# Kernel tuning notes

Hardware: AMD Instinct MI355X
Metric: run time of the kernel (lower is better)

Reference implementation:

```python
import jax, jax.numpy as jnp
import numpy as np
from jax import lax

B, L, D, N, DFF = 2, 2048, 1024, 16, 4096
EPS = 1e-6


def _phi1(z):
    # (exp(z) - 1) / z with stable limit 1 at z -> 0
    small = jnp.abs(z) < 1e-4
    zs = jnp.where(small, 1.0, z)
    return jnp.where(small, 1.0 + 0.5 * z, jnp.expm1(zs) / zs)


def _rmsnorm(x, w):
    return x * lax.rsqrt(jnp.mean(x * x, axis=-1, keepdims=True) + EPS) * w


def setup_inputs() -> dict:
    key = jax.random.key(0)
    ks = jax.random.split(key, 16)
    s_in = 0.02
    return {
        "x": jax.random.normal(ks[0], (B, L, D), jnp.float32),
        "norm1_w": jnp.ones((D,), jnp.float32),
        "norm2_w": jnp.ones((D,), jnp.float32),
        "A_log": jnp.log(jnp.arange(1, N + 1, dtype=jnp.float32)),  # A = -exp(A_log)
        "D_param": jnp.ones((D,), jnp.float32),
        "scale": jnp.ones((D,), jnp.float32),
        "Wdt": jax.random.normal(ks[1], (D, D), jnp.float32) * s_in,
        "bdt": jnp.zeros((D,), jnp.float32),
        "WB": jax.random.normal(ks[2], (N, D), jnp.float32) * s_in,
        "bB": jnp.zeros((N,), jnp.float32),
        "WC": jax.random.normal(ks[3], (N, D), jnp.float32) * s_in,
        "bC": jnp.zeros((N,), jnp.float32),
        "W1": jax.random.normal(ks[4], (DFF, D), jnp.float32) * s_in,
        "b1": jnp.zeros((DFF,), jnp.float32),
        "W2": jax.random.normal(ks[5], (D, DFF), jnp.float32) * s_in,
        "b2": jnp.zeros((D,), jnp.float32),
    }


def _mamba(xn, A_log, D_param, scale, Wdt, bdt, WB, bB, WC, bC):
    # xn: (B, L, D)
    A = -jnp.exp(A_log)  # (N,)
    dt = jax.nn.softplus(xn @ Wdt.T + bdt)      # (B, L, D)
    Bv = xn @ WB.T + bB                          # (B, L, N)
    Cv = xn @ WC.T + bC                          # (B, L, N)
    dtA = dt[..., None] * A                      # (B, L, D, N)
    dA = jnp.exp(dtA)                            # (B, L, D, N)
    b = _phi1(dtA) * Bv[:, :, None, :] * xn[..., None]  # (B, L, D, N)

    def step(h, inp):
        dA_t, b_t = inp
        h = dA_t * h + b_t
        return h, h

    h0 = jnp.zeros((xn.shape[0], xn.shape[2], A.shape[0]), xn.dtype)
    _, h_traj = lax.scan(step, h0, (jnp.moveaxis(dA, 1, 0), jnp.moveaxis(b, 1, 0)))
    h_traj = jnp.moveaxis(h_traj, 0, 1)          # (B, L, D, N)
    y = jnp.einsum('bln,bldn->bld', Cv, h_traj) + D_param * xn
    return y * scale


def reference(x, norm1_w, norm2_w, A_log, D_param, scale, Wdt, bdt, WB, bB, WC, bC, W1, b1, W2, b2):
    res = x
    xn = _rmsnorm(x, norm1_w)
    x = _mamba(xn, A_log, D_param, scale, Wdt, bdt, WB, bB, WC, bC) + res
    res = x
    xn = _rmsnorm(x, norm2_w)
    h = jax.nn.gelu(xn @ W1.T + b1, approximate=True)
    x = h @ W2.T + b2 + res
    return x
```

## Files before the change

kernel.cpp:

```cpp
#include <hip/hip_runtime.h>


#define GLOBAL_AS __attribute__((address_space(1)))
#define LDS_AS __attribute__((address_space(3)))

typedef __attribute__((ext_vector_type(8))) short short8;
typedef __attribute__((ext_vector_type(4))) float f32x4;

static constexpr int Bc = 2, Lc = 2048, Dc = 1024, Nc = 16, DFFc = 4096;
static constexpr int BL = Bc * Lc;
static constexpr int CHUNK = 32, NCHUNK = 64;
static constexpr int NP = 1152;

__device__ __forceinline__ float bf2f(unsigned short u) {
    return __uint_as_float(((unsigned)u) << 16);
}
__device__ __forceinline__ unsigned short f2bf(float f) {
    unsigned u = __float_as_uint(f);
    u += 0x7fff + ((u >> 16) & 1);
    return (unsigned short)(u >> 16);
}

static constexpr int NCVT = NP * Dc + DFFc * Dc + Dc * DFFc;
static constexpr int NCVT_BLK = NCVT / 4 / 256;
__global__ __launch_bounds__(256) void cvt_rms(const float* __restrict__ Wdt,
                                               const float* __restrict__ WB,
                                               const float* __restrict__ WC,
                                               const float* __restrict__ W1,
                                               const float* __restrict__ W2,
                                               unsigned short* __restrict__ wcomb,
                                               unsigned short* __restrict__ w1b,
                                               unsigned short* __restrict__ w2b,
                                               const float* __restrict__ x,
                                               const float* __restrict__ n1w,
                                               unsigned short* __restrict__ xn1) {
    const int tid = threadIdx.x;
    if (blockIdx.x < NCVT_BLK) {
        constexpr int n0 = Dc * Dc;
        constexpr int n1 = Nc * Dc;
        constexpr int n2 = Nc * Dc;
        constexpr int n3 = 96 * Dc;
        constexpr int nC = n0 + n1 + n2 + n3;
        constexpr int n4 = DFFc * Dc;
        constexpr int n5 = Dc * DFFc;
        static_assert(nC == NP * Dc, "pad mismatch");
        const int i = (blockIdx.x * 256 + tid) * 4;
        const float* s;
        unsigned short* d;
        if (i < n0)                 { s = Wdt + i;             d = wcomb + i; }
        else if (i < n0 + n1)       { s = WB + (i - n0);       d = wcomb + i; }
        else if (i < n0 + n1 + n2)  { s = WC + (i - n0 - n1);  d = wcomb + i; }
        else if (i < nC)            { *(ushort4*)(wcomb + i) = ushort4{0, 0, 0, 0}; return; }
        else if (i < nC + n4)       { s = W1 + (i - nC);       d = w1b + (i - nC); }
        else if (i < nC + n4 + n5)  { s = W2 + (i - nC - n4);  d = w2b + (i - nC - n4); }
        else return;
        float4 v = *(const float4*)s;
        ushort4 o;
        o.x = f2bf(v.x); o.y = f2bf(v.y); o.z = f2bf(v.z); o.w = f2bf(v.w);
        *(ushort4*)d = o;
        return;
    }
    const int row = blockIdx.x - NCVT_BLK;
    float4 v = ((const float4*)(x + (size_t)row * Dc))[tid];
    float ss = v.x * v.x + v.y * v.y + v.z * v.z + v.w * v.w;
#pragma unroll
    for (int off = 32; off > 0; off >>= 1) ss += __shfl_down(ss, off, 64);
    __shared__ float red[4];
    if ((tid & 63) == 0) red[tid >> 6] = ss;
    __syncthreads();
    float tot = red[0] + red[1] + red[2] + red[3];
    float rs = rsqrtf(tot * (1.0f / Dc) + 1e-6f);
    float4 wv = ((const float4*)n1w)[tid];
    ushort4 o;
    o.x = f2bf(v.x * rs * wv.x); o.y = f2bf(v.y * rs * wv.y);
    o.z = f2bf(v.z * rs * wv.z); o.w = f2bf(v.w * rs * wv.w);
    ((ushort4*)(xn1 + (size_t)row * Dc))[tid] = o;
}

__global__ __launch_bounds__(256) void rmsnorm_k(const float* __restrict__ x,
                                                 const float* __restrict__ w,
                                                 unsigned short* __restrict__ out) {
    const int row = blockIdx.x, tid = threadIdx.x;
    float4 v = ((const float4*)(x + (size_t)row * Dc))[tid];
    float ss = v.x * v.x + v.y * v.y + v.z * v.z + v.w * v.w;
#pragma unroll
    for (int off = 32; off > 0; off >>= 1) ss += __shfl_down(ss, off, 64);
    __shared__ float red[4];
    if ((tid & 63) == 0) red[tid >> 6] = ss;
    __syncthreads();
    float tot = red[0] + red[1] + red[2] + red[3];
    float rs = rsqrtf(tot * (1.0f / Dc) + 1e-6f);
    float4 wv = ((const float4*)w)[tid];
    ushort4 o;
    o.x = f2bf(v.x * rs * wv.x); o.y = f2bf(v.y * rs * wv.y);
    o.z = f2bf(v.z * rs * wv.z); o.w = f2bf(v.w * rs * wv.w);
    ((ushort4*)(out + (size_t)row * Dc))[tid] = o;
}

template <int TBN, int EPI, int KS>
__global__ __launch_bounds__(512)
__attribute__((amdgpu_waves_per_eu(2, 2)))
void gemm256(const unsigned short* __restrict__ A,
             const unsigned short* __restrict__ Bw,
             const float* __restrict__ bias,
             void* __restrict__ outp, int M, int N, int K) {
    constexpr int BM = 256;
    constexpr int LB = TBN / 128;
    constexpr int FN = TBN / 64;
    constexpr int FN2 = TBN / 128;
    constexpr int NQ = TBN / 8;
    constexpr int ASZ = BM * 64;
    constexpr int SLOTSZ = (BM + TBN) * 64;
    constexpr int NT = KS / 64;
    static_assert(NT % 2 == 0, "NT must be even");
    __shared__ __align__(16) unsigned short smem[2 * SLOTSZ];

    const int tid = threadIdx.x;
    const int wave = tid >> 6, lane = tid & 63;
    const int q = lane >> 4, r16 = lane & 15;
    const int wm = (wave >> 2) * 128;
    const int wn = (wave & 3) * (TBN / 4);

    const int gx = gridDim.x, gy = gridDim.y;
    int flat = blockIdx.y * gx + blockIdx.x;
    int bm, bn;
    if (gy == 16 && (gx & 1) == 0) {
        int xcd = flat & 7, idx = flat >> 3;
        int r = (xcd & 3) * 4 + (idx & 3);
        int c = (xcd >> 2) * (gx >> 1) + (idx >> 2);
        bm = r * BM; bn = c * TBN;
    } else {
        bm = (flat / gx) * BM; bn = (flat % gx) * TBN;
    }
    const int k0 = blockIdx.z * KS;

    const int srow = tid >> 3;
    const int scl = (tid & 7) ^ (srow & 7);

    auto stgA = [&](int t, int h) {
        const int sb = (t & 1) * SLOTSZ + h * 8192;
        const size_t gb = (size_t)(bm + h * 128) * K + (size_t)(k0 + t * 64 + scl * 8);
#pragma unroll
        for (int it = 0; it < 2; ++it)
            __builtin_amdgcn_global_load_lds(
                (const GLOBAL_AS void*)(A + gb + (size_t)(it * 64 + srow) * K),
                (LDS_AS void*)&smem[sb + (it * 512 + tid) * 8], 16, 0, 0);
    };
    auto stgB = [&](int t, int h) {
        const int sb = (t & 1) * SLOTSZ + ASZ + h * (TBN / 2) * 64;
        const size_t gb = (size_t)(bn + h * (TBN / 2)) * K + (size_t)(k0 + t * 64 + scl * 8);
#pragma unroll
        for (int it = 0; it < LB; ++it)
            __builtin_amdgcn_global_load_lds(
                (const GLOBAL_AS void*)(Bw + gb + (size_t)(it * 64 + srow) * K),
                (LDS_AS void*)&smem[sb + (it * 512 + tid) * 8], 16, 0, 0);
    };

    const int swz = r16 & 7;
    const int ck0 = (q ^ swz) * 8;
    const int ck1 = ((4 + q) ^ swz) * 8;

    f32x4 acc[8][FN] = {};
    short8 a[4][2], bA[FN2][2], bB[FN2][2];

#define RD_A(S, H)                                                                 \
    _Pragma("unroll") for (int i = 0; i < 4; ++i) {                                \
        const int ro = (S) * SLOTSZ + (wm + (H) * 64 + i * 16 + r16) * 64;         \
        a[i][0] = *(const short8*)&smem[ro + ck0];                                 \
        a[i][1] = *(const short8*)&smem[ro + ck1];                                 \
    }
#define RD_B(S, N2, DST)                                                           \
    _Pragma("unroll") for (int j = 0; j < FN2; ++j) {                              \
        const int ro = (S) * SLOTSZ + ASZ + (wn + (N2) * NQ + j * 16 + r16) * 64;  \
        DST[j][0] = *(const short8*)&smem[ro + ck0];                               \
        DST[j][1] = *(const short8*)&smem[ro + ck1];                               \
    }
#define MMA(H, N2, B)                                                              \
    _Pragma("unroll") for (int i = 0; i < 4; ++i)                                  \
    _Pragma("unroll") for (int j = 0; j < FN2; ++j) {                              \
        acc[(H)*4 + i][(N2)*FN2 + j] = __builtin_amdgcn_mfma_f32_16x16x32_bf16(    \
            a[i][0], B[j][0], acc[(H)*4 + i][(N2)*FN2 + j], 0, 0, 0);              \
        acc[(H)*4 + i][(N2)*FN2 + j] = __builtin_amdgcn_mfma_f32_16x16x32_bf16(    \
            a[i][1], B[j][1], acc[(H)*4 + i][(N2)*FN2 + j], 0, 0, 0);              \
    }
#define LGKM_FENCE()                                                               \
    asm volatile("s_waitcnt lgkmcnt(0)" ::: "memory");                             \
    __builtin_amdgcn_sched_barrier(0)

#define TILE(T, S)                                                                 \
    do {                                                                           \
        const int t_ = (T);                                                        \
                                                                           \
        RD_A(S, 0);                                                                \
        RD_B(S, 0, bA);                                                            \
        if (t_ + 1 < NT) stgB(t_ + 1, 1);                                          \
        __builtin_amdgcn_s_barrier();                                              \
        LGKM_FENCE();                                                              \
        __builtin_amdgcn_s_setprio(1); MMA(0, 0, bA); __builtin_amdgcn_s_setprio(0); \
        __builtin_amdgcn_s_barrier();                                              \
                                                                           \
        RD_B(S, 1, bB);                                                            \
        if (t_ + 1 < NT) stgA(t_ + 1, 1);                                          \
        __builtin_amdgcn_s_barrier();                                              \
        LGKM_FENCE();                                                              \
        __builtin_amdgcn_s_setprio(1); MMA(0, 1, bB); __builtin_amdgcn_s_setprio(0); \
        __builtin_amdgcn_s_barrier();                                              \
                                                                           \
        RD_A(S, 1);                                                                \
        if (t_ + 2 < NT) stgB(t_ + 2, 0);                                          \
        __builtin_amdgcn_s_barrier();                                              \
        LGKM_FENCE();                                                              \
        __builtin_amdgcn_s_setprio(1); MMA(1, 0, bA); __builtin_amdgcn_s_setprio(0); \
        __builtin_amdgcn_s_barrier();                                              \
                                        \
        if (t_ + 2 < NT) stgA(t_ + 2, 0);                                          \
        __builtin_amdgcn_s_setprio(1); MMA(1, 1, bB); __builtin_amdgcn_s_setprio(0); \
        if (t_ + 2 < NT) {                                                         \
            asm volatile("s_waitcnt vmcnt(%0)" ::"n"(LB + 2) : "memory");          \
        } else {                                                                   \
            asm volatile("s_waitcnt vmcnt(0)" ::: "memory");                       \
        }                                                                          \
        __builtin_amdgcn_s_barrier();                                              \
    } while (0)

    stgB(0, 0); stgA(0, 0); stgB(0, 1); stgA(0, 1);
    stgB(1, 0); stgA(1, 0);
    asm volatile("s_waitcnt vmcnt(%0)" ::"n"(LB + 2) : "memory");
    __builtin_amdgcn_s_barrier();

    for (int t2 = 0; t2 < NT; t2 += 2) {
        TILE(t2, 0);
        TILE(t2 + 1, 1);
    }
#undef TILE
#undef LGKM_FENCE
#undef MMA
#undef RD_B
#undef RD_A

    if constexpr (EPI == 1) {
#pragma unroll
        for (int hh = 0; hh < 2; ++hh) {
            __syncthreads();
            if ((wm >> 7) == hh) {
#pragma unroll
                for (int h = 0; h < 2; ++h)
#pragma unroll
                    for (int j = 0; j < FN; ++j) {
                        const int col = wn + j * 16 + r16;
                        const float bv = bias[bn + col];
#pragma unroll
                        for (int i = 0; i < 4; ++i) {
                            const int row0 = h * 64 + i * 16 + q * 4;
#pragma unroll
                            for (int rg = 0; rg < 4; ++rg) {
                                float v = acc[h * 4 + i][j][rg] + bv;
                                float uu = 0.7978845608028654f * (v + 0.044715f * v * v * v);
                                float e = __expf(2.0f * uu);
                                float t = 1.0f - 2.0f * __builtin_amdgcn_rcpf(e + 1.0f);
                                smem[(row0 + rg) * (TBN + 8) + col] = f2bf(0.5f * v * (1.0f + t));
                            }
                        }
                    }
            }
            __syncthreads();
            constexpr int CH = TBN / 8;
            constexpr int RPP = 512 / CH;
            const int ch = tid & (CH - 1), rb = tid / CH;
#pragma unroll
            for (int t = 0; t < 128 / RPP; ++t) {
                int row = rb + t * RPP;
                short8 v = *(const short8*)&smem[row * (TBN + 8) + ch * 8];
                *(short8*)&((unsigned short*)outp)[(size_t)(bm + hh * 128 + row) * N + bn + ch * 8] = v;
            }
        }
    } else {
        float* ftile = (float*)smem;
        float* po = (float*)outp + (size_t)blockIdx.z * M * N;
#pragma unroll
        for (int hh = 0; hh < 2; ++hh) {
            __syncthreads();
            if ((wm >> 7) == hh) {
#pragma unroll
                for (int h = 0; h < 2; ++h)
#pragma unroll
                    for (int j = 0; j < FN; ++j) {
                        const int col = wn + j * 16 + r16;
#pragma unroll
                        for (int i = 0; i < 4; ++i) {
                            const int row0 = h * 64 + i * 16 + q * 4;
#pragma unroll
                            for (int rg = 0; rg < 4; ++rg)
                                ftile[(row0 + rg) * (TBN + 4) + col] = acc[h * 4 + i][j][rg];
                        }
                    }
            }
            __syncthreads();
            constexpr int CH = TBN / 4;
            constexpr int RPP = 512 / CH;
            const int ch = tid & (CH - 1), rb = tid / CH;
#pragma unroll
            for (int t = 0; t < 128 / RPP; ++t) {
                int row = rb + t * RPP;
                float4 v = *(const float4*)&ftile[row * (TBN + 4) + ch * 4];
                *(float4*)&po[(size_t)(bm + hh * 128 + row) * N + bn + ch * 4] = v;
            }
        }
    }
}

__global__ __launch_bounds__(256) void ffn2_combine(const float* __restrict__ p0,
                                                    const float* __restrict__ p1,
                                                    const float* __restrict__ bias,
                                                    const float* __restrict__ res,
                                                    float* __restrict__ out) {
    int i = blockIdx.x * 256 + threadIdx.x;
    float4 a = ((const float4*)p0)[i];
    float4 b = ((const float4*)p1)[i];
    float4 r = ((const float4*)res)[i];
    float4 bb = ((const float4*)bias)[i & 255];
    float4 o;
    o.x = a.x + b.x + r.x + bb.x;
    o.y = a.y + b.y + r.y + bb.y;
    o.z = a.z + b.z + r.z + bb.z;
    o.w = a.w + b.w + r.w + bb.w;
    ((float4*)out)[i] = o;
}

__device__ __forceinline__ void dt_decode(float v, float& dt, float& r) {
    float e = __expf(-fabsf(v));
    dt = fmaxf(v, 0.0f) + log1pf(e);
    float num = (v >= 0.0f) ? e : 1.0f;
    r = num * __builtin_amdgcn_rcpf(1.0f + e);
}

__global__ __launch_bounds__(256) void scan_pass1(const float* __restrict__ Pt,
                                                  const float* __restrict__ bdt,
                                                  const float* __restrict__ bB,
                                                  const float* __restrict__ Alog,
                                                  const unsigned short* __restrict__ xn,
                                                  float* __restrict__ S,
                                                  float* __restrict__ P) {
    const int bid = blockIdx.x;
    const int dg = bid & 3, b = (bid >> 2) & 1, c = bid >> 3;
    const int tid = threadIdx.x;
    const int d = dg * 256 + tid;
    const int l0 = c * CHUNK;
    __shared__ float lBvI[CHUNK][16];
    for (int t = tid; t < CHUNK * 16; t += 256) {
        int il = t >> 4, n = t & 15;
        size_t ro = (size_t)(b * Lc + l0 + il) * NP + 1024 + n;
        float ia = __builtin_amdgcn_rcpf(__expf(Alog[n]));
        lBvI[il][n] = (Pt[ro] + bB[n]) * ia;
    }
    __syncthreads();
    float S_[16];
#pragma unroll
    for (int n = 0; n < 16; ++n) S_[n] = 0.0f;
    float rprod = 1.0f;
    const float bd = bdt[d];
    const size_t rb = (size_t)(b * Lc + l0) * NP + d;
    for (int il = 0; il < CHUNK; ++il) {
        float v = Pt[rb + (size_t)il * NP] + bd;
        float xnv = bf2f(xn[((size_t)(b * Lc + l0 + il)) * Dc + d]);
        float dt, r;
        dt_decode(v, dt, r);
        rprod *= r;
        float w = xnv * __builtin_amdgcn_rcpf(dt);
        float en = r;
#pragma unroll
        for (int n = 0; n < 16; ++n) {
            float bt = (1.0f - en) * w * lBvI[il][n];
            S_[n] = fmaf(en, S_[n], bt);
            en *= r;
        }
    }
    float pn = rprod;
    const size_t ob = ((size_t)(c * Bc + b) * Nc) * Dc + d;
#pragma unroll
    for (int n = 0; n < 16; ++n) {
        S[ob + (size_t)n * Dc] = S_[n];
        P[ob + (size_t)n * Dc] = pn;
        pn *= rprod;
    }
}

__global__ __launch_bounds__(256) void scan_pass2(const float* __restrict__ S,
                                                  const float* __restrict__ P,
                                                  float* __restrict__ carry) {
    const int t = blockIdx.x * 256 + threadIdx.x;
    float h = 0.0f;
#pragma unroll 8
    for (int c = 0; c < NCHUNK; ++c) {
        const size_t idx = (size_t)c * (Bc * Nc * Dc) + t;
        carry[idx] = h;
        h = fmaf(P[idx], h, S[idx]);
    }
}

__global__ __launch_bounds__(256) void scan_pass3(const float* __restrict__ Pt,
                                                  const float* __restrict__ bdt,
                                                  const float* __restrict__ bB,
                                                  const float* __restrict__ bC,
                                                  const float* __restrict__ Alog,
                                                  const unsigned short* __restrict__ xn,
                                                  const float* __restrict__ carry,
                                                  const float* __restrict__ x,
                                                  const float* __restrict__ Dp,
                                                  const float* __restrict__ scale,
                                                  float* __restrict__ x2) {
    const int bid = blockIdx.x;
    const int dg = bid & 3, b = (bid >> 2) & 1, c = bid >> 3;
    const int tid = threadIdx.x;
    const int d = dg * 256 + tid;
    const int l0 = c * CHUNK;
    __shared__ float lBvI[CHUNK][16];
    __shared__ float lCv[CHUNK][16];
    for (int t = tid; t < CHUNK * 16; t += 256) {
        int il = t >> 4, n = t & 15;
        size_t rowb = (size_t)(b * Lc + l0 + il) * NP;
        float ia = __builtin_amdgcn_rcpf(__expf(Alog[n]));
        lBvI[il][n] = (Pt[rowb + 1024 + n] + bB[n]) * ia;
        lCv[il][n] = Pt[rowb + 1040 + n] + bC[n];
    }
    __syncthreads();
    float h[16];
    const size_t cb = ((size_t)(c * Bc + b) * Nc) * Dc + d;
#pragma unroll
    for (int n = 0; n < 16; ++n) h[n] = carry[cb + (size_t)n * Dc];
    const float Dd = Dp[d], sc = scale[d], bd = bdt[d];
    const size_t rb = (size_t)(b * Lc + l0) * NP + d;
    const size_t xb = ((size_t)b * Lc + l0) * Dc + d;
    for (int il = 0; il < CHUNK; ++il) {
        float v = Pt[rb + (size_t)il * NP] + bd;
        float xnv = bf2f(xn[xb + (size_t)il * Dc]);
        float dt, r;
        dt_decode(v, dt, r);
        float w = xnv * __builtin_amdgcn_rcpf(dt);
        float en = r;
        float y = 0.0f;
#pragma unroll
        for (int n = 0; n < 16; ++n) {
            float bt = (1.0f - en) * w * lBvI[il][n];
            h[n] = fmaf(en, h[n], bt);
            y = fmaf(lCv[il][n], h[n], y);
            en *= r;
        }
        x2[xb + (size_t)il * Dc] = (y + Dd * xnv) * sc + x[xb + (size_t)il * Dc];
    }
}

extern "C" void kernel_launch(void* const* d_in, const int* in_sizes, int n_in,
                              void* d_out, int out_size, void* d_ws, size_t ws_size,
                              hipStream_t stream) {
    const float* x     = (const float*)d_in[0];
    const float* n1w   = (const float*)d_in[1];
    const float* n2w   = (const float*)d_in[2];
    const float* Alog  = (const float*)d_in[3];
    const float* Dp    = (const float*)d_in[4];
    const float* scale = (const float*)d_in[5];
    const float* Wdt   = (const float*)d_in[6];
    const float* bdt   = (const float*)d_in[7];
    const float* WB    = (const float*)d_in[8];
    const float* bB    = (const float*)d_in[9];
    const float* WC    = (const float*)d_in[10];
    const float* bC    = (const float*)d_in[11];
    const float* W1    = (const float*)d_in[12];
    const float* b1    = (const float*)d_in[13];
    const float* W2    = (const float*)d_in[14];
    const float* b2    = (const float*)d_in[15];
    float* out = (float*)d_out;

    char* p = (char*)d_ws;
    auto alloc = [&](size_t bytes) {
        char* r = p;
        p += (bytes + 255) & ~(size_t)255;
        return r;
    };
    const size_t MB = 1ull << 20;
    unsigned short* wcomb = (unsigned short*)alloc((size_t)NP * Dc * 2);
    unsigned short* w1b   = (unsigned short*)alloc((size_t)DFFc * Dc * 2);
    unsigned short* w2b   = (unsigned short*)alloc((size_t)Dc * DFFc * 2);
    float* x2    = (float*)alloc((size_t)BL * Dc * 4);
    unsigned short* xn2b = (unsigned short*)alloc((size_t)BL * Dc * 2);
    unsigned short* xn1b = (unsigned short*)alloc((size_t)BL * Dc * 2);
    char* region1 = alloc(36 * MB);
    float* Pt = (float*)region1;
    unsigned short* hb = (unsigned short*)region1;
    char* region2 = alloc(32 * MB);
    float* Sb    = (float*)region2;
    float* Pb    = (float*)(region2 + 8 * MB);
    float* carry = (float*)(region2 + 16 * MB);
    float* fp    = (float*)region2;

    cvt_rms<<<NCVT_BLK + BL, 256, 0, stream>>>(Wdt, WB, WC, W1, W2,
                                               wcomb, w1b, w2b, x, n1w, xn1b);

    gemm256<128, 3, 1024><<<dim3(NP / 128, BL / 256, 1), 512, 0, stream>>>(
        xn1b, wcomb, nullptr, Pt, BL, NP, Dc);

    scan_pass1<<<NCHUNK * Bc * (Dc / 256), 256, 0, stream>>>(
        Pt, bdt, bB, Alog, xn1b, Sb, Pb);
    scan_pass2<<<(Bc * Nc * Dc) / 256, 256, 0, stream>>>(Sb, Pb, carry);
    scan_pass3<<<NCHUNK * Bc * (Dc / 256), 256, 0, stream>>>(
        Pt, bdt, bB, bC, Alog, xn1b, carry, x, Dp, scale, x2);

    rmsnorm_k<<<BL, 256, 0, stream>>>(x2, n2w, xn2b);

    gemm256<256, 1, 1024><<<dim3(DFFc / 256, BL / 256, 1), 512, 0, stream>>>(
        xn2b, w1b, b1, hb, BL, DFFc, Dc);

    gemm256<128, 3, 2048><<<dim3(Dc / 128, BL / 256, 2), 512, 0, stream>>>(
        hb, w2b, nullptr, fp, BL, Dc, DFFc);

    ffn2_combine<<<(BL * Dc / 4) / 256, 256, 0, stream>>>(
        fp, fp + (size_t)BL * Dc, b2, x2, out);
}
```

Before: 312.5 us.

## Fuse scan passes and second RMSNorm into one cooperative kernel with grid syncs

Replaces the three chunked-scan kernels and the second RMSNorm kernel with a single cooperative kernel of 512 blocks, separated by grid-wide syncs. The per-step decay and input weights from pass 1 are cached in shared memory (64 KB) so pass 3 does not re-read Pt or recompute softplus and exp. This removes three launches and the repeated decode work, but adds grid-sync cost, uses only 512 blocks for the carry pass, and depends on all blocks being co-resident.

```diff
diff --git a/kernel.cpp b/kernel.cpp
--- a/kernel.cpp
+++ b/kernel.cpp
@@ -1,4 +1,7 @@
 #include <hip/hip_runtime.h>
+#include <hip/hip_cooperative_groups.h>
+
+namespace cg = cooperative_groups;
 
 
 #define GLOBAL_AS __attribute__((address_space(1)))
@@ -77,26 +80,6 @@
     ((ushort4*)(xn1 + (size_t)row * Dc))[tid] = o;
 }
 
-__global__ __launch_bounds__(256) void rmsnorm_k(const float* __restrict__ x,
-                                                 const float* __restrict__ w,
-                                                 unsigned short* __restrict__ out) {
-    const int row = blockIdx.x, tid = threadIdx.x;
-    float4 v = ((const float4*)(x + (size_t)row * Dc))[tid];
-    float ss = v.x * v.x + v.y * v.y + v.z * v.z + v.w * v.w;
-#pragma unroll
-    for (int off = 32; off > 0; off >>= 1) ss += __shfl_down(ss, off, 64);
-    __shared__ float red[4];
-    if ((tid & 63) == 0) red[tid >> 6] = ss;
-    __syncthreads();
-    float tot = red[0] + red[1] + red[2] + red[3];
-    float rs = rsqrtf(tot * (1.0f / Dc) + 1e-6f);
-    float4 wv = ((const float4*)w)[tid];
-    ushort4 o;
-    o.x = f2bf(v.x * rs * wv.x); o.y = f2bf(v.y * rs * wv.y);
-    o.z = f2bf(v.z * rs * wv.z); o.w = f2bf(v.w * rs * wv.w);
-    ((ushort4*)(out + (size_t)row * Dc))[tid] = o;
-}
-
 template <int TBN, int EPI, int KS>
 __global__ __launch_bounds__(512)
 __attribute__((amdgpu_waves_per_eu(2, 2)))
@@ -334,88 +317,29 @@
     r = num * __builtin_amdgcn_rcpf(1.0f + e);
 }
 
-__global__ __launch_bounds__(256) void scan_pass1(const float* __restrict__ Pt,
-                                                  const float* __restrict__ bdt,
-                                                  const float* __restrict__ bB,
-                                                  const float* __restrict__ Alog,
-                                                  const unsigned short* __restrict__ xn,
-                                                  float* __restrict__ S,
-                                                  float* __restrict__ P) {
+__global__ __launch_bounds__(256) void scan_fused(
+    const float* __restrict__ Pt, const float* __restrict__ bdt,
+    const float* __restrict__ bB, const float* __restrict__ bC,
+    const float* __restrict__ Alog, const unsigned short* __restrict__ xn,
+    const float* __restrict__ x, const float* __restrict__ Dp,
+    const float* __restrict__ scale, const float* __restrict__ n2w,
+    float* __restrict__ S, float* __restrict__ P, float* __restrict__ carry,
+    float* __restrict__ x2, unsigned short* __restrict__ xn2) {
+    __shared__ float lw[CHUNK][256];
+    __shared__ float lr[CHUNK][256];
+    __shared__ float lBvI[CHUNK][16];
+    __shared__ float lCv[CHUNK][16];
+    __shared__ float red[4];
+
+    cg::grid_group grid = cg::this_grid();
+
     const int bid = blockIdx.x;
     const int dg = bid & 3, b = (bid >> 2) & 1, c = bid >> 3;
     const int tid = threadIdx.x;
     const int d = dg * 256 + tid;
     const int l0 = c * CHUNK;
-    __shared__ float lBvI[CHUNK][16];
-    for (int t = tid; t < CHUNK * 16; t += 256) {
-        int il = t >> 4, n = t & 15;
-        size_t ro = (size_t)(b * Lc + l0 + il) * NP + 1024 + n;
-        float ia = __builtin_amdgcn_rcpf(__expf(Alog[n]));
-        lBvI[il][n] = (Pt[ro] + bB[n]) * ia;
-    }
-    __syncthreads();
-    float S_[16];
-#pragma unroll
-    for (int n = 0; n < 16; ++n) S_[n] = 0.0f;
-    float rprod = 1.0f;
-    const float bd = bdt[d];
-    const size_t rb = (size_t)(b * Lc + l0) * NP + d;
-    for (int il = 0; il < CHUNK; ++il) {
-        float v = Pt[rb + (size_t)il * NP] + bd;
-        float xnv = bf2f(xn[((size_t)(b * Lc + l0 + il)) * Dc + d]);
-        float dt, r;
-        dt_decode(v, dt, r);
-        rprod *= r;
-        float w = xnv * __builtin_amdgcn_rcpf(dt);
-        float en = r;
-#pragma unroll
-        for (int n = 0; n < 16; ++n) {
-            float bt = (1.0f - en) * w * lBvI[il][n];
-            S_[n] = fmaf(en, S_[n], bt);
-            en *= r;
-        }
-    }
-    float pn = rprod;
-    const size_t ob = ((size_t)(c * Bc + b) * Nc) * Dc + d;
-#pragma unroll
-    for (int n = 0; n < 16; ++n) {
-        S[ob + (size_t)n * Dc] = S_[n];
-        P[ob + (size_t)n * Dc] = pn;
-        pn *= rprod;
-    }
-}
-
-__global__ __launch_bounds__(256) void scan_pass2(const float* __restrict__ S,
-                                                  const float* __restrict__ P,
-                                                  float* __restrict__ carry) {
-    const int t = blockIdx.x * 256 + threadIdx.x;
-    float h = 0.0f;
-#pragma unroll 8
-    for (int c = 0; c < NCHUNK; ++c) {
-        const size_t idx = (size_t)c * (Bc * Nc * Dc) + t;
-        carry[idx] = h;
-        h = fmaf(P[idx], h, S[idx]);
-    }
-}
-
-__global__ __launch_bounds__(256) void scan_pass3(const float* __restrict__ Pt,
-                                                  const float* __restrict__ bdt,
-                                                  const float* __restrict__ bB,
-                                                  const float* __restrict__ bC,
-                                                  const float* __restrict__ Alog,
-                                                  const unsigned short* __restrict__ xn,
-                                                  const float* __restrict__ carry,
-                                                  const float* __restrict__ x,
-                                                  const float* __restrict__ Dp,
-                                                  const float* __restrict__ scale,
-                                                  float* __restrict__ x2) {
-    const int bid = blockIdx.x;
-    const int dg = bid & 3, b = (bid >> 2) & 1, c = bid >> 3;
-    const int tid = threadIdx.x;
-    const int d = dg * 256 + tid;
-    const int l0 = c * CHUNK;
-    __shared__ float lBvI[CHUNK][16];
-    __shared__ float lCv[CHUNK][16];
+    const size_t xb = ((size_t)b * Lc + l0) * Dc + d;
+
     for (int t = tid; t < CHUNK * 16; t += 256) {
         int il = t >> 4, n = t & 15;
         size_t rowb = (size_t)(b * Lc + l0 + il) * NP;
@@ -424,29 +348,96 @@
         lCv[il][n] = Pt[rowb + 1040 + n] + bC[n];
     }
     __syncthreads();
-    float h[16];
-    const size_t cb = ((size_t)(c * Bc + b) * Nc) * Dc + d;
-#pragma unroll
-    for (int n = 0; n < 16; ++n) h[n] = carry[cb + (size_t)n * Dc];
-    const float Dd = Dp[d], sc = scale[d], bd = bdt[d];
-    const size_t rb = (size_t)(b * Lc + l0) * NP + d;
-    const size_t xb = ((size_t)b * Lc + l0) * Dc + d;
-    for (int il = 0; il < CHUNK; ++il) {
-        float v = Pt[rb + (size_t)il * NP] + bd;
-        float xnv = bf2f(xn[xb + (size_t)il * Dc]);
-        float dt, r;
-        dt_decode(v, dt, r);
-        float w = xnv * __builtin_amdgcn_rcpf(dt);
-        float en = r;
-        float y = 0.0f;
+
+    {
+        float S_[16];
+#pragma unroll
+        for (int n = 0; n < 16; ++n) S_[n] = 0.0f;
+        float rprod = 1.0f;
+        const float bd = bdt[d];
+        const size_t rb = (size_t)(b * Lc + l0) * NP + d;
+        for (int il = 0; il < CHUNK; ++il) {
+            float v = Pt[rb + (size_t)il * NP] + bd;
+            float xnv = bf2f(xn[xb + (size_t)il * Dc]);
+            float dt, r;
+            dt_decode(v, dt, r);
+            float w = xnv * __builtin_amdgcn_rcpf(dt);
+            lw[il][tid] = w;
+            lr[il][tid] = r;
+            rprod *= r;
+            float en = r;
+#pragma unroll
+            for (int n = 0; n < 16; ++n) {
+                float bt = (1.0f - en) * w * lBvI[il][n];
+                S_[n] = fmaf(en, S_[n], bt);
+                en *= r;
+            }
+        }
+        float pn = rprod;
+        const size_t ob = ((size_t)(c * Bc + b) * Nc) * Dc + d;
 #pragma unroll
         for (int n = 0; n < 16; ++n) {
-            float bt = (1.0f - en) * w * lBvI[il][n];
-            h[n] = fmaf(en, h[n], bt);
-            y = fmaf(lCv[il][n], h[n], y);
-            en *= r;
+            S[ob + (size_t)n * Dc] = S_[n];
+            P[ob + (size_t)n * Dc] = pn;
+            pn *= rprod;
         }
-        x2[xb + (size_t)il * Dc] = (y + Dd * xnv) * sc + x[xb + (size_t)il * Dc];
+    }
+    __threadfence();
+    grid.sync();
+
+    if (bid < (Bc * Nc * Dc) / 256) {
+        const int t = bid * 256 + tid;
+        float h = 0.0f;
+#pragma unroll 8
+        for (int cc = 0; cc < NCHUNK; ++cc) {
+            const size_t idx = (size_t)cc * (Bc * Nc * Dc) + t;
+            carry[idx] = h;
+            h = fmaf(P[idx], h, S[idx]);
+        }
+    }
+    __threadfence();
+    grid.sync();
+
+    {
+        float h[16];
+        const size_t cb = ((size_t)(c * Bc + b) * Nc) * Dc + d;
+#pragma unroll
+        for (int n = 0; n < 16; ++n) h[n] = carry[cb + (size_t)n * Dc];
+        const float Dd = Dp[d], sc = scale[d];
+        for (int il = 0; il < CHUNK; ++il) {
+            float w = lw[il][tid], r = lr[il][tid];
+            float xnv = bf2f(xn[xb + (size_t)il * Dc]);
+            float en = r;
+            float y = 0.0f;
+#pragma unroll
+            for (int n = 0; n < 16; ++n) {
+                float bt = (1.0f - en) * w * lBvI[il][n];
+                h[n] = fmaf(en, h[n], bt);
+                y = fmaf(lCv[il][n], h[n], y);
+                en *= r;
+            }
+            x2[xb + (size_t)il * Dc] = (y + Dd * xnv) * sc + x[xb + (size_t)il * Dc];
+        }
+    }
+    __threadfence();
+    grid.sync();
+
+    for (int rr = 0; rr < 8; ++rr) {
+        const int row = bid * 8 + rr;
+        float4 v = ((const float4*)(x2 + (size_t)row * Dc))[tid];
+        float ss = v.x * v.x + v.y * v.y + v.z * v.z + v.w * v.w;
+#pragma unroll
+        for (int off = 32; off > 0; off >>= 1) ss += __shfl_down(ss, off, 64);
+        if ((tid & 63) == 0) red[tid >> 6] = ss;
+        __syncthreads();
+        float tot = red[0] + red[1] + red[2] + red[3];
+        float rs = rsqrtf(tot * (1.0f / Dc) + 1e-6f);
+        float4 wv = ((const float4*)n2w)[tid];
+        ushort4 o;
+        o.x = f2bf(v.x * rs * wv.x); o.y = f2bf(v.y * rs * wv.y);
+        o.z = f2bf(v.z * rs * wv.z); o.w = f2bf(v.w * rs * wv.w);
+        ((ushort4*)(xn2 + (size_t)row * Dc))[tid] = o;
+        __syncthreads();
     }
 }
 
@@ -499,13 +490,14 @@
     gemm256<128, 3, 1024><<<dim3(NP / 128, BL / 256, 1), 512, 0, stream>>>(
         xn1b, wcomb, nullptr, Pt, BL, NP, Dc);
 
-    scan_pass1<<<NCHUNK * Bc * (Dc / 256), 256, 0, stream>>>(
-        Pt, bdt, bB, Alog, xn1b, Sb, Pb);
-    scan_pass2<<<(Bc * Nc * Dc) / 256, 256, 0, stream>>>(Sb, Pb, carry);
-    scan_pass3<<<NCHUNK * Bc * (Dc / 256), 256, 0, stream>>>(
-        Pt, bdt, bB, bC, Alog, xn1b, carry, x, Dp, scale, x2);
-
-    rmsnorm_k<<<BL, 256, 0, stream>>>(x2, n2w, xn2b);
+    {
+        void* args[] = {(void*)&Pt,   (void*)&bdt,   (void*)&bB,    (void*)&bC,
+                        (void*)&Alog, (void*)&xn1b,  (void*)&x,     (void*)&Dp,
+                        (void*)&scale,(void*)&n2w,   (void*)&Sb,    (void*)&Pb,
+                        (void*)&carry,(void*)&x2,    (void*)&xn2b};
+        hipLaunchCooperativeKernel(reinterpret_cast<void*>(scan_fused),
+                                   dim3(512), dim3(256), args, 0, stream);
+    }
 
     gemm256<256, 1, 1024><<<dim3(DFFc / 256, BL / 256, 1), 512, 0, stream>>>(
         xn2b, w1b, b1, hb, BL, DFFc, Dc);
```

New measurement: 640.8 us. 2.05x slower.
